# Kernel tuning notes

Measured on AMD Instinct MI355X. Metric: run time of the kernel, lower is better.

Reference implementation:

```python
import jax, jax.numpy as jnp
import numpy as np
from itertools import product

N = 300000          # active voxels
CIN, C = 16, 32     # input / conv channels
K = 27              # 3x3x3 kernel volume
Z, Y, X = 41, 1024, 1024  # sparse spatial shape (grid_size[::-1] + [1,0,0])
B = 2               # batch size
EPS = 1e-3          # BatchNorm eps (matches norm_fn eps=0.001)


def _build_coords_and_rulebook(rng):
    # unique active coords per batch element
    total = Z * Y * X
    per = N // B
    coords = []
    for b in range(B):
        lin = np.unique(rng.integers(0, total, size=int(per * 1.3)))
        rng.shuffle(lin)
        lin = lin[:per]
        assert lin.shape[0] == per
        z = lin // (Y * X)
        y = (lin % (Y * X)) // X
        x = lin % X
        coords.append(np.stack([np.full(per, b), z, y, x], axis=1))
    coords = np.concatenate(coords, axis=0).astype(np.int64)  # [N,4]

    # hash-free rulebook via sorted linear keys + searchsorted
    key = ((coords[:, 0] * Z + coords[:, 1]) * Y + coords[:, 2]) * X + coords[:, 3]
    perm = np.argsort(key)
    skey = key[perm]
    nbr = np.full((N, K), -1, dtype=np.int32)
    bz, zz, yy, xx = coords[:, 0], coords[:, 1], coords[:, 2], coords[:, 3]
    for k, (dz, dy, dx) in enumerate(product((-1, 0, 1), repeat=3)):
        nz, ny, nx = zz + dz, yy + dy, xx + dx
        valid = (nz >= 0) & (nz < Z) & (ny >= 0) & (ny < Y) & (nx >= 0) & (nx < X)
        nkey = ((bz * Z + nz) * Y + ny) * X + nx
        pos = np.searchsorted(skey, nkey)
        pos = np.clip(pos, 0, N - 1)
        found = valid & (skey[pos] == nkey)
        nbr[:, k] = np.where(found, perm[pos], -1).astype(np.int32)
    return coords, nbr


def _bn_params(k, c):
    k1, k2, k3, k4 = jax.random.split(k, 4)
    gamma = jax.random.uniform(k1, (c,), minval=0.5, maxval=1.5)
    beta = jax.random.normal(k2, (c,)) * 0.1
    mean = jax.random.normal(k3, (c,)) * 0.1
    var = jax.random.uniform(k4, (c,), minval=0.5, maxval=1.5)
    return jnp.stack([gamma, beta, mean, var], axis=0)  # [4,C]


def setup_inputs() -> dict:
    rng = np.random.default_rng(0)
    _, nbr = _build_coords_and_rulebook(rng)

    key = jax.random.key(0)
    ks = jax.random.split(key, 12)
    feat = jax.random.normal(ks[0], (N, CIN), dtype=jnp.float32)

    def conv_w(k, cin, cout):
        return jax.random.normal(k, (K, cin, cout), dtype=jnp.float32) * (1.0 / np.sqrt(K * cin))

    return {
        "voxel_features": feat,
        "neighbor_idx": jnp.asarray(nbr),
        "w_in": conv_w(ks[1], CIN, C), "bn_in": _bn_params(ks[2], C),
        "w1a": conv_w(ks[3], C, C), "bn1a": _bn_params(ks[4], C),
        "w1b": conv_w(ks[5], C, C), "bn1b": _bn_params(ks[6], C),
        "w2a": conv_w(ks[7], C, C), "bn2a": _bn_params(ks[8], C),
        "w2b": conv_w(ks[9], C, C), "bn2b": _bn_params(ks[10], C),
    }


def reference(voxel_features, neighbor_idx, w_in, bn_in, w1a, bn1a, w1b, bn1b,
              w2a, bn2a, w2b, bn2b):
    def bn(x, p):
        gamma, beta, mean, var = p
        return gamma * (x - mean) * jax.lax.rsqrt(var + EPS) + beta

    def subm(feat, w):
        # submanifold conv: gather active neighbors, GEMM per kernel offset, accumulate
        out = jnp.zeros((feat.shape[0], w.shape[2]), feat.dtype)
        for k in range(K):
            idx = neighbor_idx[:, k]
            g = jnp.where((idx >= 0)[:, None], feat[jnp.maximum(idx, 0)], 0.0)
            out = out + g @ w[k]
        return out

    # conv_input: SubMConv3d + BN + ReLU
    x = jax.nn.relu(bn(subm(voxel_features, w_in), bn_in))
    # conv1: two SparseBasicBlocks (conv-bn-relu-conv-bn + residual, relu)
    for wa, bna, wb, bnb in ((w1a, bn1a, w1b, bn1b), (w2a, bn2a, w2b, bn2b)):
        identity = x
        x = jax.nn.relu(bn(subm(x, wa), bna))
        x = bn(subm(x, wb), bnb)
        x = jax.nn.relu(x + identity)
    # voxel importance (vis_importance branch, minus file IO / sorting side effects)
    voxel_importance = jax.nn.sigmoid(jnp.mean(jnp.abs(x), axis=1, keepdims=True))
    return x, voxel_importance
```

## Files before the change

### kernel.cpp

```cpp
#include <hip/hip_runtime.h>
#include <hip/hip_bf16.h>
#include <hip/hip_fp16.h>
#include <cstdint>
#include <cstddef>

#define NVOX 300000
#define KNBR 27
#define COUT 32
#define CINP 32
#define NT   (NVOX / 16)
#define RB   ((NVOX + 255) / 256)
#define WFIXE (5 * KNBR * CINP * COUT)
#define WFB  ((WFIXE + 255) / 256)
#define WDE  (5 * COUT * CINP)
#define WDB  ((WDE + 255) / 256)
#define WDK  (5 * KNBR * CINP * COUT)
#define WKB  ((WDK + 255) / 256)
#define WPL  (KNBR * CINP * COUT)
#define GD   1984
#define GF0  64
#define GC0  512
#define GP   256
#define PCAP 150016

typedef __hip_bfloat16 bf16;
typedef _Float16 half8 __attribute__((ext_vector_type(8)));
typedef float floatx4 __attribute__((ext_vector_type(4)));
typedef unsigned short ushort8 __attribute__((ext_vector_type(8)));

__device__ __forceinline__ float bf2f(unsigned short u) {
    union { unsigned int i; float f; } x; x.i = ((unsigned int)u) << 16; return x.f;
}
__device__ __forceinline__ int detect_fp32(const void* b0) {
    const unsigned short* p = (const unsigned short*)b0;
    int hits = 0;
    for (int i = 0; i < 16; i++) {
        float v = bf2f(p[2 * i]);
        if (v >= 0.25f && v <= 4.0f) hits++;
    }
    return (hits >= 8) ? 0 : 1;
}
__device__ __forceinline__ float rdw(const void* w, int rel, int fp32) {
    return fp32 ? ((const float*)w)[rel] : __bfloat162float(((const bf16*)w)[rel]);
}


__global__ __launch_bounds__(256)
void setup_kernel(const int* __restrict__ nbr,
                  const void* w0, const void* w1, const void* w2, const void* w3, const void* w4,
                  const void* b0, const void* b1, const void* b2, const void* b3, const void* b4,
                  float* __restrict__ wfix, __half* __restrict__ wtf, __half* __restrict__ wtk,
                  float* __restrict__ bnab,
                  int* __restrict__ flag, int* __restrict__ counter,
                  int* __restrict__ cvlist, int* __restrict__ corrpos,
                  unsigned char* __restrict__ nnarr, int* __restrict__ pk1) {
    const int tid = threadIdx.x;

    if (blockIdx.x < RB) {
        __shared__ int flags[256];
        __shared__ int pk1s[256];
        __shared__ int wsum[4];
        __shared__ int wbase[4];
        flags[tid] = 0;
        __syncthreads();
        const int base = blockIdx.x * 256;
        const int nvox = (NVOX - base < 256) ? (NVOX - base) : 256;
        const int nI4  = (nvox * KNBR) >> 2;
        const int4* p4 = (const int4*)(nbr + (size_t)base * KNBR);
        for (int i = tid; i < nI4; i += 256) {
            const int4 q = p4[i];
            if ((q.x & q.y & q.z & q.w) < 0) continue;
            const unsigned t = (unsigned)(i << 2);
            if (q.x >= 0) { unsigned u = t;     unsigned lv = (u * 4855u) >> 17; unsigned kk = u - lv * 27u; if (kk != 13u) { atomicAdd(&flags[lv], 1); pk1s[lv] = (int)((kk << 19) | (unsigned)q.x); } }
            if (q.y >= 0) { unsigned u = t + 1; unsigned lv = (u * 4855u) >> 17; unsigned kk = u - lv * 27u; if (kk != 13u) { atomicAdd(&flags[lv], 1); pk1s[lv] = (int)((kk << 19) | (unsigned)q.y); } }
            if (q.z >= 0) { unsigned u = t + 2; unsigned lv = (u * 4855u) >> 17; unsigned kk = u - lv * 27u; if (kk != 13u) { atomicAdd(&flags[lv], 1); pk1s[lv] = (int)((kk << 19) | (unsigned)q.z); } }
            if (q.w >= 0) { unsigned u = t + 3; unsigned lv = (u * 4855u) >> 17; unsigned kk = u - lv * 27u; if (kk != 13u) { atomicAdd(&flags[lv], 1); pk1s[lv] = (int)((kk << 19) | (unsigned)q.w); } }
        }
        __syncthreads();
        const int v = base + tid;
        const int nn = flags[tid];
        const bool inr = (tid < nvox);
        if (inr) nnarr[v] = (unsigned char)(nn > 255 ? 255 : nn);
        if (inr && nn == 1) pk1[v] = pk1s[tid];
        const bool f = inr && (nn > 0);
        const unsigned long long wm = __ballot(f);
        const int wd = tid >> 6, ln = tid & 63;
        if (ln == 0) wsum[wd] = __popcll(wm);
        __syncthreads();
        if (tid == 0) {
            int t0 = wsum[0], t1 = wsum[1], t2 = wsum[2], t3 = wsum[3];
            int tot = t0 + t1 + t2 + t3;
            int b = tot ? atomicAdd(counter, tot) : 0;
            wbase[0] = b; wbase[1] = b + t0; wbase[2] = b + t0 + t1; wbase[3] = b + t0 + t1 + t2;
        }
        __syncthreads();
        if (f) {
            int pos = wbase[wd] + __popcll(wm & ((1ULL << ln) - 1ULL));
            cvlist[pos] = v;
            corrpos[v]  = pos;
        }
        return;
    }

    const int fp32 = detect_fp32(b0);

    if (blockIdx.x < RB + WFB) {
        int i = (blockIdx.x - RB) * 256 + tid;
        if (i >= WFIXE) return;
        int L   = i / (KNBR * CINP * COUT);
        int rem = i % (KNBR * CINP * COUT);
        int k   = rem / (CINP * COUT);
        int kk  = (rem / COUT) % CINP;
        int nn  = rem % COUT;
        const void* w = (L == 0) ? w0 : (L == 1) ? w1 : (L == 2) ? w2 : (L == 3) ? w3 : w4;
        int cinL = (L == 0) ? 16 : 32;
        wfix[i] = (kk < cinL) ? rdw(w, (k * cinL + kk) * COUT + nn, fp32) : 0.f;
        return;
    }

    if (blockIdx.x < RB + WFB + WDB) {
        int i = (blockIdx.x - RB - WFB) * 256 + tid;
        if (i >= WDE) return;
        int L  = i / (COUT * CINP);
        int nn = (i / CINP) % COUT;
        int kk = i % CINP;
        const void* w = (L == 0) ? w0 : (L == 1) ? w1 : (L == 2) ? w2 : (L == 3) ? w3 : w4;
        int cinL = (L == 0) ? 16 : 32;
        int sk = (L == 0) ? kk : ((kk & 1) ? 16 + (kk >> 1) : (kk >> 1));
        float val = (sk < cinL) ? rdw(w, (13 * cinL + sk) * COUT + nn, fp32) : 0.f;
        wtf[i] = __float2half(val);
        return;
    }

    if (blockIdx.x < RB + WFB + WDB + WKB) {
        int i = (blockIdx.x - RB - WFB - WDB) * 256 + tid;
        if (i >= WDK) return;
        int L   = i / (KNBR * CINP * COUT);
        int rem = i % (KNBR * CINP * COUT);
        int k   = rem / (CINP * COUT);
        int nn  = (rem / CINP) % COUT;
        int kk  = rem % CINP;
        const void* w = (L == 0) ? w0 : (L == 1) ? w1 : (L == 2) ? w2 : (L == 3) ? w3 : w4;
        int cinL = (L == 0) ? 16 : 32;
        int sk = (L == 0) ? kk : ((kk & 1) ? 16 + (kk >> 1) : (kk >> 1));
        float val = (sk < cinL) ? rdw(w, (k * cinL + sk) * COUT + nn, fp32) : 0.f;
        wtk[i] = __float2half(val);
        return;
    }

    if (tid == 192) *flag = fp32;
    if (tid < 160) {
        int L = tid / 32, c = tid % 32;
        const void* b = (L == 0) ? b0 : (L == 1) ? b1 : (L == 2) ? b2 : (L == 3) ? b3 : b4;
        float g, be, m, v;
        if (fp32) {
            const float* q = (const float*)b;
            g = q[c]; be = q[32 + c]; m = q[64 + c]; v = q[96 + c];
        } else {
            const bf16* q = (const bf16*)b;
            g = __bfloat162float(q[c]); be = __bfloat162float(q[32 + c]);
            m = __bfloat162float(q[64 + c]); v = __bfloat162float(q[96 + c]);
        }
        float a = g * rsqrtf(v + 1e-3f);
        bnab[L * 64 + c]      = a;
        bnab[L * 64 + 32 + c] = be - a * m;
    }
}


struct DW {
    half8 wa[5], wb[5];
    float ba[5], bb[5], bc[5], bd[5];
};
__device__ __forceinline__ void load_dw(DW& d, const __half* __restrict__ wtf,
                                        const float* __restrict__ bnab, int n, int quad) {
#pragma unroll
    for (int L = 0; L < 5; L++) {
        d.wa[L] = *(const half8*)((const _Float16*)wtf + L * 1024 + n * 32 + quad * 8);
        d.wb[L] = *(const half8*)((const _Float16*)wtf + L * 1024 + (n + 16) * 32 + quad * 8);
        d.ba[L] = bnab[L * 64 + n];      d.bb[L] = bnab[L * 64 + 32 + n];
        d.bc[L] = bnab[L * 64 + 16 + n]; d.bd[L] = bnab[L * 64 + 48 + n];
    }
}

__device__ __forceinline__ void dense_range(
    int gw, int nw, const DW& dw,
    const void* __restrict__ feat, int fp32, void* __restrict__ out_base,
    _Float16 (* __restrict__ myT)[40], int n, int quad) {
    for (int t = gw; t < NT; t += nw) {
        const int v0 = t * 16;
        half8 af = {};
        if (quad < 2) {
            if (fp32) {
                const float* p = (const float*)feat + (size_t)(v0 + n) * 16 + quad * 8;
                const float4 u0 = *(const float4*)p;
                const float4 u1 = *(const float4*)(p + 4);
                af[0] = (_Float16)u0.x; af[1] = (_Float16)u0.y; af[2] = (_Float16)u0.z; af[3] = (_Float16)u0.w;
                af[4] = (_Float16)u1.x; af[5] = (_Float16)u1.y; af[6] = (_Float16)u1.z; af[7] = (_Float16)u1.w;
            } else {
                const ushort8 u = *(const ushort8*)((const unsigned short*)feat + (size_t)(v0 + n) * 16 + quad * 8);
#pragma unroll
                for (int j = 0; j < 8; j++) af[j] = (_Float16)bf2f(u[j]);
            }
        }
        float id0[4], id1[4];
#pragma unroll
        for (int L = 0; L < 5; L++) {
            floatx4 c0 = {0.f, 0.f, 0.f, 0.f}, c1 = {0.f, 0.f, 0.f, 0.f};
            c0 = __builtin_amdgcn_mfma_f32_16x16x32_f16(af, dw.wa[L], c0, 0, 0, 0);
            c1 = __builtin_amdgcn_mfma_f32_16x16x32_f16(af, dw.wb[L], c1, 0, 0, 0);
            if (L < 4) {
#pragma unroll
                for (int r = 0; r < 4; r++) {
                    float y0 = fmaf(dw.ba[L], c0[r], dw.bb[L]);
                    float y1 = fmaf(dw.bc[L], c1[r], dw.bd[L]);
                    if (L == 2) { y0 += id0[r]; y1 += id1[r]; }
                    y0 = fmaxf(y0, 0.f); y1 = fmaxf(y1, 0.f);
                    if (L == 0 || L == 2) { id0[r] = y0; id1[r] = y1; }
                    const int m = quad * 4 + r;
                    *reinterpret_cast<__half2*>(&myT[m][2 * n]) = __floats2half2_rn(y0, y1);
                }
                af = *reinterpret_cast<const half8*>(&myT[n][quad * 8]);
            } else {
#pragma unroll
                for (int r = 0; r < 4; r++) {
                    float y0 = fmaxf(fmaf(dw.ba[4], c0[r], dw.bb[4]) + id0[r], 0.f);
                    float y1 = fmaxf(fmaf(dw.bc[4], c1[r], dw.bd[4]) + id1[r], 0.f);
                    const int v = v0 + quad * 4 + r;
                    float s = y0 + y1;
#pragma unroll
                    for (int o = 1; o < 16; o <<= 1) s += __shfl_xor(s, o, 16);
                    const float imp = 1.0f / (1.0f + expf(-s * (1.0f / 32.0f)));
                    if (fp32) {
                        float* ox = (float*)out_base;
                        ox[(size_t)v * COUT + n]      = y0;
                        ox[(size_t)v * COUT + n + 16] = y1;
                        if (n == 0) ox[(size_t)NVOX * COUT + v] = imp;
                    } else {
                        bf16* ox = (bf16*)out_base;
                        ox[(size_t)v * COUT + n]      = __float2bfloat16(y0);
                        ox[(size_t)v * COUT + n + 16] = __float2bfloat16(y1);
                        if (n == 0) ox[(size_t)NVOX * COUT + v] = __float2bfloat16(imp);
                    }
                }
            }
        }
    }
}

__device__ __forceinline__ void classify_range(
    int nC, int wbase0, int wstride, int lane,
    const int* __restrict__ cvlist,
    const unsigned char* __restrict__ nnarr, const int* __restrict__ pk1,
    int* __restrict__ clist, int* __restrict__ ccount,
    int* __restrict__ pbuck, int* __restrict__ pcnt13) {
    for (int i0 = wbase0; i0 < nC; i0 += wstride) {
        const int i = i0 + lane;
        const bool inr = i < nC;
        int v = 0; bool pair = false; int u = 0, k = 0;
        if (inr) {
            v = cvlist[i];
            if (nnarr[v] == 1) {
                const int e = pk1[v];
                u = e & 0x7FFFF; k = e >> 19;
                pair = (nnarr[u] == 1);
            }
        }
        const bool emitP = pair && (k < 13);
#pragma unroll
        for (int bb = 0; bb < 13; bb++) {
            const unsigned long long mb = __ballot(emitP && (k == bb));
            if (mb == 0) continue;
            int basep = 0;
            if (lane == 0) basep = atomicAdd(&pcnt13[bb * 16], __popcll(mb));
            basep = __shfl(basep, 0, 64);
            if (emitP && (k == bb)) {
                const int pos = basep + __popcll(mb & ((1ULL << lane) - 1ULL));
                int* pb = pbuck + (size_t)bb * (2 * PCAP);
                pb[2 * pos]     = (v << 5) | k;
                pb[2 * pos + 1] = u;
            }
        }
        const bool cplx = inr && !pair;
        const unsigned long long mc = __ballot(cplx);
        const int cc = __popcll(mc);
        int baseC = 0;
        if (lane == 0 && cc) baseC = atomicAdd(ccount, cc);
        baseC = __shfl(baseC, 0, 64);
        if (cplx) clist[baseC + __popcll(mc & ((1ULL << lane) - 1ULL))] = i;
    }
}

__device__ __forceinline__ void cplx0_range(
    int gw, int nw, int lane,
    const void* __restrict__ feat, const int* __restrict__ nbr,
    const int* __restrict__ cvlist, const int* __restrict__ corrpos,
    const int* __restrict__ clist, const int* __restrict__ ccount,
    int* __restrict__ ctap,
    const float* __restrict__ wt, const float* __restrict__ bnab,
    __half* __restrict__ xout, int fp32) {
    const int c = lane & 31;
    const int nC = *ccount;
    const float bna = bnab[c], bnb = bnab[32 + c];
    for (int jj = gw; jj < nC; jj += nw) {
        const int ii = clist[jj];
        const int vv = cvlist[ii];
        int idx = (lane < KNBR) ? nbr[(size_t)vv * KNBR + lane] : -1;
        const bool valid = idx >= 0;
        unsigned long long m = __ballot(valid) & ((1ULL << KNBR) - 1ULL);
        if (valid) {
            int sp  = corrpos[idx];
            int pos = __popcll(m & ((1ULL << lane) - 1ULL));
            ctap[(size_t)ii * 28 + 1 + pos] = (sp << 5) | lane;
        }
        if (lane == 0) ctap[(size_t)ii * 28] = __popcll(m);
        float acc0 = 0.f, acc1 = 0.f;
        while (m) {
            const int k0 = (int)__builtin_ctzll(m); m &= m - 1;
            int k1 = -1;
            if (m) { k1 = (int)__builtin_ctzll(m); m &= m - 1; }
            const int kme = (lane >= 32) ? k1 : k0;
            const bool act = (kme >= 0);
            const int kk = act ? kme : 0;
            const int src = __shfl(idx, kk, 64);
            float xv = 0.f;
            if (act && c < 16)
                xv = fp32 ? ((const float*)feat)[(size_t)src * 16 + c]
                          : bf2f(((const unsigned short*)feat)[(size_t)src * 16 + c]);
            const float* wk = wt + (size_t)kk * (CINP * COUT) + c;
#pragma unroll
            for (int j = 0; j < 16; j += 2) {
                float xa = __shfl(xv, j, 32);
                float xb = __shfl(xv, j + 1, 32);
                acc0 = fmaf(xa, wk[j * COUT], acc0);
                acc1 = fmaf(xb, wk[(j + 1) * COUT], acc1);
            }
        }
        float acc = acc0 + acc1;
        acc += __shfl_xor(acc, 32, 64);
        float y = fmaxf(fmaf(bna, acc, bnb), 0.f);
        if (lane < 32) xout[(size_t)ii * COUT + c] = __float2half(y);
    }
}

template<int HAS_RES>
__device__ __forceinline__ void fixs_range(
    int gw, int nw, int lane,
    const __half* __restrict__ xin, const int* __restrict__ ctap,
    const int* __restrict__ clist, const int* __restrict__ ccount,
    const float* __restrict__ wt, const float* __restrict__ bnab,
    const __half* __restrict__ res, __half* __restrict__ xout) {
    const int c = lane & 31;
    const int nC = *ccount;
    const float bna = bnab[c], bnb = bnab[32 + c];
    for (int jj = gw; jj < nC; jj += nw) {
        const int i = clist[jj];
        const size_t tb = (size_t)i * 28;
        const int cnt = ctap[tb];
        const int tp  = ctap[tb + 1 + lane];
        float acc0 = 0.f, acc1 = 0.f;
        for (int t = 0; t < cnt; t += 2) {
            const bool actB = (t + 1) < cnt;
            const int sel = (lane >= 32 && actB) ? (t + 1) : t;
            const int tap = __shfl(tp, sel, 64);
            const bool act = (lane < 32) || actB;
            const int sp = tap >> 5, kk = tap & 31;
            const float xv = act ? __half2float(xin[(size_t)sp * COUT + c]) : 0.f;
            const float* wk = wt + (size_t)kk * (CINP * COUT) + c;
#pragma unroll
            for (int j = 0; j < 32; j += 2) {
                acc0 = fmaf(__shfl(xv, j, 32),     wk[j * COUT],       acc0);
                acc1 = fmaf(__shfl(xv, j + 1, 32), wk[(j + 1) * COUT], acc1);
            }
        }
        float acc = acc0 + acc1;
        acc += __shfl_xor(acc, 32, 64);
        float y = fmaf(bna, acc, bnb);
        if (HAS_RES) y += __half2float(res[(size_t)i * COUT + c]);
        y = fmaxf(y, 0.f);
        if (lane < 32) xout[(size_t)i * COUT + c] = __float2half(y);
    }
}

__device__ __forceinline__ void pairs_range(
    int gw, int nw, int lane,
    const void* __restrict__ feat,
    const int* __restrict__ pcnt13, const int* __restrict__ pbuck,
    const __half* __restrict__ wtk, const float* __restrict__ bnab,
    void* __restrict__ out_base, int fp32,
    _Float16 (* __restrict__ Tv)[40], _Float16 (* __restrict__ Tu)[40]) {
    const int n = lane & 15, quad = lane >> 4;
    int G = 0;
#pragma unroll
    for (int bb = 0; bb < 13; bb++) G += (pcnt13[bb * 16] + 15) >> 4;

    for (int gi = gw; gi < G; gi += nw) {
        int b = 0, g = 0, nb = 0;
        {
            int acc = 0, found = 0;
#pragma unroll
            for (int bb = 0; bb < 13; bb++) {
                const int cbb = pcnt13[bb * 16];
                const int ng = (cbb + 15) >> 4;
                if (!found && gi < acc + ng) { b = bb; g = gi - acc; nb = cbb; found = 1; }
                acc += ng;
            }
        }
        const int* pb = pbuck + (size_t)b * (2 * PCAP);
        const int base = g * 16;
        int rA = base + n; if (rA > nb - 1) rA = nb - 1;
        const int vA = pb[2 * rA] >> 5;
        const int uA = pb[2 * rA + 1];

        half8 afv = {}, afu = {};
        if (quad < 2) {
            if (fp32) {
                const float* pv = (const float*)feat + (size_t)vA * 16 + quad * 8;
                const float* pu = (const float*)feat + (size_t)uA * 16 + quad * 8;
                const float4 v0 = *(const float4*)pv, v1 = *(const float4*)(pv + 4);
                const float4 u0 = *(const float4*)pu, u1 = *(const float4*)(pu + 4);
                afv[0] = (_Float16)v0.x; afv[1] = (_Float16)v0.y; afv[2] = (_Float16)v0.z; afv[3] = (_Float16)v0.w;
                afv[4] = (_Float16)v1.x; afv[5] = (_Float16)v1.y; afv[6] = (_Float16)v1.z; afv[7] = (_Float16)v1.w;
                afu[0] = (_Float16)u0.x; afu[1] = (_Float16)u0.y; afu[2] = (_Float16)u0.z; afu[3] = (_Float16)u0.w;
                afu[4] = (_Float16)u1.x; afu[5] = (_Float16)u1.y; afu[6] = (_Float16)u1.z; afu[7] = (_Float16)u1.w;
            } else {
                const ushort8 sv = *(const ushort8*)((const unsigned short*)feat + (size_t)vA * 16 + quad * 8);
                const ushort8 su = *(const ushort8*)((const unsigned short*)feat + (size_t)uA * 16 + quad * 8);
#pragma unroll
                for (int j = 0; j < 8; j++) { afv[j] = (_Float16)bf2f(sv[j]); afu[j] = (_Float16)bf2f(su[j]); }
            }
        }
        float idv0[4], idv1[4], idu0[4], idu1[4];
#pragma unroll
        for (int L = 0; L < 5; L++) {
            const _Float16* w13 = (const _Float16*)wtk + (size_t)(L * 27 + 13) * 1024;
            const _Float16* wkb = (const _Float16*)wtk + (size_t)(L * 27 + b) * 1024;
            const _Float16* wqb = (const _Float16*)wtk + (size_t)(L * 27 + (26 - b)) * 1024;
            const half8 B13a = *(const half8*)(w13 + n * 32 + quad * 8);
            const half8 B13b = *(const half8*)(w13 + (n + 16) * 32 + quad * 8);
            const half8 Bka  = *(const half8*)(wkb + n * 32 + quad * 8);
            const half8 Bkb  = *(const half8*)(wkb + (n + 16) * 32 + quad * 8);
            const half8 Bqa  = *(const half8*)(wqb + n * 32 + quad * 8);
            const half8 Bqb  = *(const half8*)(wqb + (n + 16) * 32 + quad * 8);
            const float a0 = bnab[L * 64 + n],      c0b = bnab[L * 64 + 32 + n];
            const float a1 = bnab[L * 64 + 16 + n], c1b = bnab[L * 64 + 48 + n];
            floatx4 cv0 = {0.f,0.f,0.f,0.f}, cv1 = {0.f,0.f,0.f,0.f};
            floatx4 cu0 = {0.f,0.f,0.f,0.f}, cu1 = {0.f,0.f,0.f,0.f};
            cv0 = __builtin_amdgcn_mfma_f32_16x16x32_f16(afv, B13a, cv0, 0, 0, 0);
            cv0 = __builtin_amdgcn_mfma_f32_16x16x32_f16(afu, Bka,  cv0, 0, 0, 0);
            cv1 = __builtin_amdgcn_mfma_f32_16x16x32_f16(afv, B13b, cv1, 0, 0, 0);
            cv1 = __builtin_amdgcn_mfma_f32_16x16x32_f16(afu, Bkb,  cv1, 0, 0, 0);
            cu0 = __builtin_amdgcn_mfma_f32_16x16x32_f16(afu, B13a, cu0, 0, 0, 0);
            cu0 = __builtin_amdgcn_mfma_f32_16x16x32_f16(afv, Bqa,  cu0, 0, 0, 0);
            cu1 = __builtin_amdgcn_mfma_f32_16x16x32_f16(afu, B13b, cu1, 0, 0, 0);
            cu1 = __builtin_amdgcn_mfma_f32_16x16x32_f16(afv, Bqb,  cu1, 0, 0, 0);
            if (L < 4) {
#pragma unroll
                for (int r = 0; r < 4; r++) {
                    float yv0 = fmaf(a0, cv0[r], c0b), yv1 = fmaf(a1, cv1[r], c1b);
                    float yu0 = fmaf(a0, cu0[r], c0b), yu1 = fmaf(a1, cu1[r], c1b);
                    if (L == 2) { yv0 += idv0[r]; yv1 += idv1[r]; yu0 += idu0[r]; yu1 += idu1[r]; }
                    yv0 = fmaxf(yv0, 0.f); yv1 = fmaxf(yv1, 0.f);
                    yu0 = fmaxf(yu0, 0.f); yu1 = fmaxf(yu1, 0.f);
                    if (L == 0 || L == 2) { idv0[r] = yv0; idv1[r] = yv1; idu0[r] = yu0; idu1[r] = yu1; }
                    const int m = quad * 4 + r;
                    *reinterpret_cast<__half2*>(&Tv[m][2 * n]) = __floats2half2_rn(yv0, yv1);
                    *reinterpret_cast<__half2*>(&Tu[m][2 * n]) = __floats2half2_rn(yu0, yu1);
                }
                afv = *reinterpret_cast<const half8*>(&Tv[n][quad * 8]);
                afu = *reinterpret_cast<const half8*>(&Tu[n][quad * 8]);
            } else {
#pragma unroll
                for (int r = 0; r < 4; r++) {
                    const int m = quad * 4 + r;
                    const int im = base + m;
                    const bool valid = im < nb;
                    const int ri = valid ? im : (nb - 1);
                    const int vm = pb[2 * ri] >> 5;
                    const int um = pb[2 * ri + 1];
                    float yv0 = fmaxf(fmaf(a0, cv0[r], c0b) + idv0[r], 0.f);
                    float yv1 = fmaxf(fmaf(a1, cv1[r], c1b) + idv1[r], 0.f);
                    float yu0 = fmaxf(fmaf(a0, cu0[r], c0b) + idu0[r], 0.f);
                    float yu1 = fmaxf(fmaf(a1, cu1[r], c1b) + idu1[r], 0.f);
                    float sv = yv0 + yv1, su = yu0 + yu1;
#pragma unroll
                    for (int o = 1; o < 16; o <<= 1) { sv += __shfl_xor(sv, o, 16); su += __shfl_xor(su, o, 16); }
                    const float impv = 1.0f / (1.0f + expf(-sv * (1.0f / 32.0f)));
                    const float impu = 1.0f / (1.0f + expf(-su * (1.0f / 32.0f)));
                    if (valid) {
                        if (fp32) {
                            float* ox = (float*)out_base;
                            ox[(size_t)vm * COUT + n]      = yv0;
                            ox[(size_t)vm * COUT + n + 16] = yv1;
                            ox[(size_t)um * COUT + n]      = yu0;
                            ox[(size_t)um * COUT + n + 16] = yu1;
                            if (n == 0) { ox[(size_t)NVOX * COUT + vm] = impv; ox[(size_t)NVOX * COUT + um] = impu; }
                        } else {
                            bf16* ox = (bf16*)out_base;
                            ox[(size_t)vm * COUT + n]      = __float2bfloat16(yv0);
                            ox[(size_t)vm * COUT + n + 16] = __float2bfloat16(yv1);
                            ox[(size_t)um * COUT + n]      = __float2bfloat16(yu0);
                            ox[(size_t)um * COUT + n + 16] = __float2bfloat16(yu1);
                            if (n == 0) { ox[(size_t)NVOX * COUT + vm] = __float2bfloat16(impv); ox[(size_t)NVOX * COUT + um] = __float2bfloat16(impu); }
                        }
                    }
                }
            }
        }
    }
}


__global__ __launch_bounds__(256)
void phase0_kernel(const void* __restrict__ feat,
                   const int* __restrict__ cvlist,
                   const unsigned char* __restrict__ nnarr, const int* __restrict__ pk1,
                   const int* __restrict__ counter,
                   int* __restrict__ clist, int* __restrict__ ccount,
                   int* __restrict__ pbuck, int* __restrict__ pcnt13,
                   const __half* __restrict__ wtf, const float* __restrict__ bnab,
                   void* __restrict__ out_base, const int* __restrict__ flag) {
    __shared__ __align__(16) _Float16 ldsT[4][16][40];
    const int lane = threadIdx.x & 63;
    const int fp32 = *flag;
    if (blockIdx.x < GD) {
        const int gw = (blockIdx.x * 256 + threadIdx.x) >> 6;
        const int nw = (GD * 256) >> 6;
        const int wv = threadIdx.x >> 6;
        const int n = lane & 15, quad = lane >> 4;
        DW dw; load_dw(dw, wtf, bnab, n, quad);
        dense_range(gw, nw, dw, feat, fp32, out_base, ldsT[wv], n, quad);
    } else {
        const int wb = (blockIdx.x - GD) * 256 + (threadIdx.x & ~63);
        classify_range(*counter, wb, GF0 * 256, lane, cvlist, nnarr, pk1,
                       clist, ccount, pbuck, pcnt13);
    }
}

__global__ __launch_bounds__(256)
void stage1_kernel(const void* __restrict__ feat, const int* __restrict__ nbr,
                   const int* __restrict__ cvlist, const int* __restrict__ corrpos,
                   const int* __restrict__ clist, const int* __restrict__ ccount,
                   int* __restrict__ ctap,
                   const int* __restrict__ pcnt13, const int* __restrict__ pbuck,
                   const __half* __restrict__ wtk,
                   const float* __restrict__ wfixL0, const float* __restrict__ bnabL0,
                   const float* __restrict__ bnab,
                   __half* __restrict__ Xc0, void* __restrict__ out_base,
                   const int* __restrict__ flag) {
    __shared__ __align__(16) _Float16 T[4][2][16][40];
    const int lane = threadIdx.x & 63;
    const int fp32 = *flag;
    if (blockIdx.x < GC0) {
        const int gw = (blockIdx.x * 256 + threadIdx.x) >> 6;
        const int nw = (GC0 * 256) >> 6;
        cplx0_range(gw, nw, lane, feat, nbr, cvlist, corrpos, clist, ccount,
                    ctap, wfixL0, bnabL0, Xc0, fp32);
    } else {
        const int gw = ((blockIdx.x - GC0) * 256 + threadIdx.x) >> 6;
        const int nw = (GP * 256) >> 6;
        const int wv = threadIdx.x >> 6;
        pairs_range(gw, nw, lane, feat, pcnt13, pbuck, wtk, bnab,
                    out_base, fp32, T[wv][0], T[wv][1]);
    }
}

template<int HAS_RES>
__global__ __launch_bounds__(256)
void fixs_kernel(const __half* __restrict__ xin, const int* __restrict__ ctap,
                 const int* __restrict__ clist, const int* __restrict__ ccount,
                 const float* __restrict__ wt, const float* __restrict__ bnab,
                 const __half* __restrict__ res, __half* __restrict__ xout) {
    const int gw   = (blockIdx.x * 256 + threadIdx.x) >> 6;
    const int nw   = (gridDim.x * 256) >> 6;
    const int lane = threadIdx.x & 63;
    fixs_range<HAS_RES>(gw, nw, lane, xin, ctap, clist, ccount, wt, bnab, res, xout);
}

__global__ __launch_bounds__(256)
void final_kernel(const int* __restrict__ clist, const int* __restrict__ ccount,
                  const int* __restrict__ ctap, const int* __restrict__ cvlist,
                  const __half* __restrict__ Xc1, const __half* __restrict__ Xc2,
                  const float* __restrict__ wfix, const float* __restrict__ bnab,
                  void* __restrict__ out_base, const int* __restrict__ flag) {
    const int gw   = (blockIdx.x * 256 + threadIdx.x) >> 6;
    const int nw   = (gridDim.x * 256) >> 6;
    const int lane = threadIdx.x & 63;
    const int c    = lane & 31;
    const int ncplx = *ccount;
    const int fp32io = *flag;

    for (int j = gw; j < ncplx; j += nw) {
        const int i = clist[j];
        const size_t tb = (size_t)i * 28;
        const int cnt = ctap[tb];
        const int tp  = ctap[tb + 1 + lane];
        const float* wt = wfix + 4 * WPL;
        float acc0 = 0.f, acc1 = 0.f;
        for (int t = 0; t < cnt; t += 2) {
            const bool actB = (t + 1) < cnt;
            const int sel = (lane >= 32 && actB) ? (t + 1) : t;
            const int tap = __shfl(tp, sel, 64);
            const bool act = (lane < 32) || actB;
            const int sp = tap >> 5, kk = tap & 31;
            const float xv = act ? __half2float(Xc1[(size_t)sp * COUT + c]) : 0.f;
            const float* wk = wt + (size_t)kk * (CINP * COUT) + c;
#pragma unroll
            for (int jq = 0; jq < 32; jq += 2) {
                acc0 = fmaf(__shfl(xv, jq, 32),     wk[jq * COUT],       acc0);
                acc1 = fmaf(__shfl(xv, jq + 1, 32), wk[(jq + 1) * COUT], acc1);
            }
        }
        float acc = acc0 + acc1;
        acc += __shfl_xor(acc, 32, 64);
        float y = fmaf(bnab[4 * 64 + c], acc, bnab[4 * 64 + 32 + c]);
        y += __half2float(Xc2[(size_t)i * COUT + c]);
        y = fmaxf(y, 0.f);
        float s2 = y;
#pragma unroll
        for (int o = 16; o > 0; o >>= 1) s2 += __shfl_xor(s2, o, 32);
        const float imp = 1.0f / (1.0f + expf(-s2 * (1.0f / 32.0f)));
        const int v = cvlist[i];
        if (fp32io) {
            float* ox = (float*)out_base;
            if (lane < 32) ox[(size_t)v * COUT + c] = y;
            if (lane == 0) ox[(size_t)NVOX * COUT + v] = imp;
        } else {
            bf16* ox = (bf16*)out_base;
            if (lane < 32) ox[(size_t)v * COUT + c] = __float2bfloat16(y);
            if (lane == 0) ox[(size_t)NVOX * COUT + v] = __float2bfloat16(imp);
        }
    }
}

extern "C" void kernel_launch(void* const* d_in, const int* in_sizes, int n_in,
                              void* d_out, int out_size, void* d_ws, size_t ws_size,
                              hipStream_t stream) {
    char* ws = (char*)d_ws;
    int*    counter = (int*)ws;
    int*    flag    = counter + 1;
    int*    ccount  = counter + 3;
    int*    pcnt13  = (int*)(ws + 256);
    int*    cvlist  = (int*)(ws + 1280);
    int*    corrpos = cvlist + NVOX;
    int*    clist   = corrpos + NVOX;
    int*    pk1     = clist + NVOX;
    unsigned char* nnarr = (unsigned char*)(pk1 + NVOX);
    uintptr_t pa    = (((uintptr_t)(nnarr + NVOX)) + 255) & ~(uintptr_t)255;
    int*    ctap    = (int*)pa;
    int*    pbuck   = ctap + (size_t)NVOX * 28 + 64;
    float*  wfix    = (float*)(pbuck + (size_t)13 * PCAP * 2);
    float*  bnab    = wfix + WFIXE;
    __half* wtf     = (__half*)(bnab + 320);
    __half* wtk     = wtf + WDE;
    uintptr_t xa    = (((uintptr_t)(wtk + WDK)) + 255) & ~(uintptr_t)255;
    __half* Xc0 = (__half*)xa;
    __half* Xc1 = Xc0 + (size_t)NVOX * COUT;
    __half* Xc2 = Xc1 + (size_t)NVOX * COUT;

    const void* feat = d_in[0];
    const int*  nbr  = (const int*)d_in[1];

    hipMemsetAsync(ws, 0, 1088, stream);

    setup_kernel<<<dim3(RB + WFB + WDB + WKB + 1), 256, 0, stream>>>(
        nbr, d_in[2], d_in[4], d_in[6], d_in[8], d_in[10],
        d_in[3], d_in[5], d_in[7], d_in[9], d_in[11],
        wfix, wtf, wtk, bnab, flag, counter, cvlist, corrpos, nnarr, pk1);

    phase0_kernel<<<dim3(GD + GF0), 256, 0, stream>>>(
        feat, cvlist, nnarr, pk1, counter, clist, ccount, pbuck, pcnt13,
        wtf, bnab, d_out, flag);

    stage1_kernel<<<dim3(GC0 + GP), 256, 0, stream>>>(
        feat, nbr, cvlist, corrpos, clist, ccount, ctap, pcnt13, pbuck, wtk,
        wfix + 0 * WPL, bnab + 0 * 64, bnab, Xc0, d_out, flag);

    dim3 gs(512);
    fixs_kernel<0><<<gs, 256, 0, stream>>>(Xc0, ctap, clist, ccount, wfix + 1 * WPL, bnab + 1 * 64, nullptr, Xc1);
    fixs_kernel<1><<<gs, 256, 0, stream>>>(Xc1, ctap, clist, ccount, wfix + 2 * WPL, bnab + 2 * 64, Xc0, Xc2);
    fixs_kernel<0><<<gs, 256, 0, stream>>>(Xc2, ctap, clist, ccount, wfix + 3 * WPL, bnab + 3 * 64, nullptr, Xc1);

    final_kernel<<<dim3(512), 256, 0, stream>>>(
        clist, ccount, ctap, cvlist, Xc1, Xc2, wfix, bnab, d_out, flag);
}
```

Measured before the change: 191.5 us.

## Overlap neighbor-count scan with dense-voxel compute, split classify into own kernel

The rulebook scan that counts neighbors per voxel moves out of the setup kernel and into the phase0 kernel, where it runs in extra blocks alongside the dense isolated-voxel compute. Classification, which depends on that scan, becomes its own small kernel launched afterward. The setup kernel now only reformats weights. The aim is to run the memory-heavy neighbor scan concurrently with the dense compute instead of serially before it. The cost is one extra kernel launch, and phase0 now needs more shared memory per block.

```diff
diff --git a/kernel.cpp b/kernel.cpp
--- a/kernel.cpp
+++ b/kernel.cpp
@@ -18,7 +18,7 @@
 #define WKB  ((WDK + 255) / 256)
 #define WPL  (KNBR * CINP * COUT)
 #define GD   1984
-#define GF0  64
+#define GCL  64
 #define GC0  512
 #define GP   256
 #define PCAP 150016
@@ -46,66 +46,15 @@
 
 
 __global__ __launch_bounds__(256)
-void setup_kernel(const int* __restrict__ nbr,
-                  const void* w0, const void* w1, const void* w2, const void* w3, const void* w4,
-                  const void* b0, const void* b1, const void* b2, const void* b3, const void* b4,
-                  float* __restrict__ wfix, __half* __restrict__ wtf, __half* __restrict__ wtk,
-                  float* __restrict__ bnab,
-                  int* __restrict__ flag, int* __restrict__ counter,
-                  int* __restrict__ cvlist, int* __restrict__ corrpos,
-                  unsigned char* __restrict__ nnarr, int* __restrict__ pk1) {
+void setupw_kernel(const void* w0, const void* w1, const void* w2, const void* w3, const void* w4,
+                   const void* b0, const void* b1, const void* b2, const void* b3, const void* b4,
+                   float* __restrict__ wfix, __half* __restrict__ wtf, __half* __restrict__ wtk,
+                   float* __restrict__ bnab, int* __restrict__ flag) {
     const int tid = threadIdx.x;
-
-    if (blockIdx.x < RB) {
-        __shared__ int flags[256];
-        __shared__ int pk1s[256];
-        __shared__ int wsum[4];
-        __shared__ int wbase[4];
-        flags[tid] = 0;
-        __syncthreads();
-        const int base = blockIdx.x * 256;
-        const int nvox = (NVOX - base < 256) ? (NVOX - base) : 256;
-        const int nI4  = (nvox * KNBR) >> 2;
-        const int4* p4 = (const int4*)(nbr + (size_t)base * KNBR);
-        for (int i = tid; i < nI4; i += 256) {
-            const int4 q = p4[i];
-            if ((q.x & q.y & q.z & q.w) < 0) continue;
-            const unsigned t = (unsigned)(i << 2);
-            if (q.x >= 0) { unsigned u = t;     unsigned lv = (u * 4855u) >> 17; unsigned kk = u - lv * 27u; if (kk != 13u) { atomicAdd(&flags[lv], 1); pk1s[lv] = (int)((kk << 19) | (unsigned)q.x); } }
-            if (q.y >= 0) { unsigned u = t + 1; unsigned lv = (u * 4855u) >> 17; unsigned kk = u - lv * 27u; if (kk != 13u) { atomicAdd(&flags[lv], 1); pk1s[lv] = (int)((kk << 19) | (unsigned)q.y); } }
-            if (q.z >= 0) { unsigned u = t + 2; unsigned lv = (u * 4855u) >> 17; unsigned kk = u - lv * 27u; if (kk != 13u) { atomicAdd(&flags[lv], 1); pk1s[lv] = (int)((kk << 19) | (unsigned)q.z); } }
-            if (q.w >= 0) { unsigned u = t + 3; unsigned lv = (u * 4855u) >> 17; unsigned kk = u - lv * 27u; if (kk != 13u) { atomicAdd(&flags[lv], 1); pk1s[lv] = (int)((kk << 19) | (unsigned)q.w); } }
-        }
-        __syncthreads();
-        const int v = base + tid;
-        const int nn = flags[tid];
-        const bool inr = (tid < nvox);
-        if (inr) nnarr[v] = (unsigned char)(nn > 255 ? 255 : nn);
-        if (inr && nn == 1) pk1[v] = pk1s[tid];
-        const bool f = inr && (nn > 0);
-        const unsigned long long wm = __ballot(f);
-        const int wd = tid >> 6, ln = tid & 63;
-        if (ln == 0) wsum[wd] = __popcll(wm);
-        __syncthreads();
-        if (tid == 0) {
-            int t0 = wsum[0], t1 = wsum[1], t2 = wsum[2], t3 = wsum[3];
-            int tot = t0 + t1 + t2 + t3;
-            int b = tot ? atomicAdd(counter, tot) : 0;
-            wbase[0] = b; wbase[1] = b + t0; wbase[2] = b + t0 + t1; wbase[3] = b + t0 + t1 + t2;
-        }
-        __syncthreads();
-        if (f) {
-            int pos = wbase[wd] + __popcll(wm & ((1ULL << ln) - 1ULL));
-            cvlist[pos] = v;
-            corrpos[v]  = pos;
-        }
-        return;
-    }
-
     const int fp32 = detect_fp32(b0);
 
-    if (blockIdx.x < RB + WFB) {
-        int i = (blockIdx.x - RB) * 256 + tid;
+    if (blockIdx.x < WFB) {
+        int i = blockIdx.x * 256 + tid;
         if (i >= WFIXE) return;
         int L   = i / (KNBR * CINP * COUT);
         int rem = i % (KNBR * CINP * COUT);
@@ -118,8 +67,8 @@
         return;
     }
 
-    if (blockIdx.x < RB + WFB + WDB) {
-        int i = (blockIdx.x - RB - WFB) * 256 + tid;
+    if (blockIdx.x < WFB + WDB) {
+        int i = (blockIdx.x - WFB) * 256 + tid;
         if (i >= WDE) return;
         int L  = i / (COUT * CINP);
         int nn = (i / CINP) % COUT;
@@ -132,8 +81,8 @@
         return;
     }
 
-    if (blockIdx.x < RB + WFB + WDB + WKB) {
-        int i = (blockIdx.x - RB - WFB - WDB) * 256 + tid;
+    if (blockIdx.x < WFB + WDB + WKB) {
+        int i = (blockIdx.x - WFB - WDB) * 256 + tid;
         if (i >= WDK) return;
         int L   = i / (KNBR * CINP * COUT);
         int rem = i % (KNBR * CINP * COUT);
@@ -512,29 +461,80 @@
 
 
 __global__ __launch_bounds__(256)
-void phase0_kernel(const void* __restrict__ feat,
-                   const int* __restrict__ cvlist,
-                   const unsigned char* __restrict__ nnarr, const int* __restrict__ pk1,
-                   const int* __restrict__ counter,
-                   int* __restrict__ clist, int* __restrict__ ccount,
-                   int* __restrict__ pbuck, int* __restrict__ pcnt13,
+void phase0_kernel(const void* __restrict__ feat, const int* __restrict__ nbr,
+                   int* __restrict__ counter,
+                   int* __restrict__ cvlist, int* __restrict__ corrpos,
+                   unsigned char* __restrict__ nnarr, int* __restrict__ pk1,
                    const __half* __restrict__ wtf, const float* __restrict__ bnab,
                    void* __restrict__ out_base, const int* __restrict__ flag) {
     __shared__ __align__(16) _Float16 ldsT[4][16][40];
-    const int lane = threadIdx.x & 63;
-    const int fp32 = *flag;
+    __shared__ int sflags[256];
+    __shared__ int spk1[256];
+    __shared__ int swsum[4];
+    __shared__ int swbase[4];
+    const int tid  = threadIdx.x;
+    const int lane = tid & 63;
     if (blockIdx.x < GD) {
-        const int gw = (blockIdx.x * 256 + threadIdx.x) >> 6;
+        const int fp32 = *flag;
+        const int gw = (blockIdx.x * 256 + tid) >> 6;
         const int nw = (GD * 256) >> 6;
-        const int wv = threadIdx.x >> 6;
+        const int wv = tid >> 6;
         const int n = lane & 15, quad = lane >> 4;
         DW dw; load_dw(dw, wtf, bnab, n, quad);
         dense_range(gw, nw, dw, feat, fp32, out_base, ldsT[wv], n, quad);
     } else {
-        const int wb = (blockIdx.x - GD) * 256 + (threadIdx.x & ~63);
-        classify_range(*counter, wb, GF0 * 256, lane, cvlist, nnarr, pk1,
-                       clist, ccount, pbuck, pcnt13);
-    }
+        const int bi = blockIdx.x - GD;
+        sflags[tid] = 0;
+        __syncthreads();
+        const int base = bi * 256;
+        const int nvox = (NVOX - base < 256) ? (NVOX - base) : 256;
+        const int nI4  = (nvox * KNBR) >> 2;
+        const int4* p4 = (const int4*)(nbr + (size_t)base * KNBR);
+        for (int i = tid; i < nI4; i += 256) {
+            const int4 q = p4[i];
+            if ((q.x & q.y & q.z & q.w) < 0) continue;
+            const unsigned t = (unsigned)(i << 2);
+            if (q.x >= 0) { unsigned u = t;     unsigned lv = (u * 4855u) >> 17; unsigned kk = u - lv * 27u; if (kk != 13u) { atomicAdd(&sflags[lv], 1); spk1[lv] = (int)((kk << 19) | (unsigned)q.x); } }
+            if (q.y >= 0) { unsigned u = t + 1; unsigned lv = (u * 4855u) >> 17; unsigned kk = u - lv * 27u; if (kk != 13u) { atomicAdd(&sflags[lv], 1); spk1[lv] = (int)((kk << 19) | (unsigned)q.y); } }
+            if (q.z >= 0) { unsigned u = t + 2; unsigned lv = (u * 4855u) >> 17; unsigned kk = u - lv * 27u; if (kk != 13u) { atomicAdd(&sflags[lv], 1); spk1[lv] = (int)((kk << 19) | (unsigned)q.z); } }
+            if (q.w >= 0) { unsigned u = t + 3; unsigned lv = (u * 4855u) >> 17; unsigned kk = u - lv * 27u; if (kk != 13u) { atomicAdd(&sflags[lv], 1); spk1[lv] = (int)((kk << 19) | (unsigned)q.w); } }
+        }
+        __syncthreads();
+        const int v = base + tid;
+        const int nn = sflags[tid];
+        const bool inr = (tid < nvox);
+        if (inr) nnarr[v] = (unsigned char)(nn > 255 ? 255 : nn);
+        if (inr && nn == 1) pk1[v] = spk1[tid];
+        const bool f = inr && (nn > 0);
+        const unsigned long long wm = __ballot(f);
+        const int wd = tid >> 6, ln = tid & 63;
+        if (ln == 0) swsum[wd] = __popcll(wm);
+        __syncthreads();
+        if (tid == 0) {
+            int t0 = swsum[0], t1 = swsum[1], t2 = swsum[2], t3 = swsum[3];
+            int tot = t0 + t1 + t2 + t3;
+            int b = tot ? atomicAdd(counter, tot) : 0;
+            swbase[0] = b; swbase[1] = b + t0; swbase[2] = b + t0 + t1; swbase[3] = b + t0 + t1 + t2;
+        }
+        __syncthreads();
+        if (f) {
+            int pos = swbase[wd] + __popcll(wm & ((1ULL << ln) - 1ULL));
+            cvlist[pos] = v;
+            corrpos[v]  = pos;
+        }
+    }
+}
+
+__global__ __launch_bounds__(256)
+void classify_kernel(const int* __restrict__ cvlist,
+                     const unsigned char* __restrict__ nnarr, const int* __restrict__ pk1,
+                     const int* __restrict__ counter,
+                     int* __restrict__ clist, int* __restrict__ ccount,
+                     int* __restrict__ pbuck, int* __restrict__ pcnt13) {
+    const int lane = threadIdx.x & 63;
+    const int wb = blockIdx.x * 256 + (threadIdx.x & ~63);
+    classify_range(*counter, wb, GCL * 256, lane, cvlist, nnarr, pk1,
+                   clist, ccount, pbuck, pcnt13);
 }
 
 __global__ __launch_bounds__(256)
@@ -663,14 +663,17 @@
 
     hipMemsetAsync(ws, 0, 1088, stream);
 
-    setup_kernel<<<dim3(RB + WFB + WDB + WKB + 1), 256, 0, stream>>>(
-        nbr, d_in[2], d_in[4], d_in[6], d_in[8], d_in[10],
+    setupw_kernel<<<dim3(WFB + WDB + WKB + 1), 256, 0, stream>>>(
+        d_in[2], d_in[4], d_in[6], d_in[8], d_in[10],
         d_in[3], d_in[5], d_in[7], d_in[9], d_in[11],
-        wfix, wtf, wtk, bnab, flag, counter, cvlist, corrpos, nnarr, pk1);
-
-    phase0_kernel<<<dim3(GD + GF0), 256, 0, stream>>>(
-        feat, cvlist, nnarr, pk1, counter, clist, ccount, pbuck, pcnt13,
+        wfix, wtf, wtk, bnab, flag);
+
+    phase0_kernel<<<dim3(GD + RB), 256, 0, stream>>>(
+        feat, nbr, counter, cvlist, corrpos, nnarr, pk1,
         wtf, bnab, d_out, flag);
+
+    classify_kernel<<<dim3(GCL), 256, 0, stream>>>(
+        cvlist, nnarr, pk1, counter, clist, ccount, pbuck, pcnt13);
 
     stage1_kernel<<<dim3(GC0 + GP), 256, 0, stream>>>(
         feat, nbr, cvlist, corrpos, clist, ccount, ctap, pcnt13, pbuck, wtk,
```

Result: slower. 202.9 us (+5.9%).
